# Kernel tuning notes

Measured on AMD Instinct MI355X. Metric: run time of the kernel, lower is better.

Reference implementation:

```python
import jax, jax.numpy as jnp
import numpy as np

B, E, H, W, HEADS = 2, 128, 64, 64, 4
FUSED = 2 * E + 1          # concat fusion: C_state + C_trigger + 1 (gnn context)
FC = FUSED // 2            # 128 fusion output channels (= AttentionMIL feature_dim)
EPS = 1e-5
NEG = -1e9


def _conv(x, w, b=None, pad=0):
    out = jax.lax.conv_general_dilated(x, w, (1, 1), [(pad, pad), (pad, pad)],
                                       dimension_numbers=('NCHW', 'OIHW', 'NCHW'))
    return out if b is None else out + b[None, :, None, None]


def _bn(x, g, b):
    # training-mode batchnorm (batch statistics), matching torch default mode
    m = x.mean((0, 2, 3), keepdims=True)
    v = x.var((0, 2, 3), keepdims=True)
    return g[None, :, None, None] * (x - m) * jax.lax.rsqrt(v + EPS) + b[None, :, None, None]


def _mha(q_in, kv_in, w_qkv, b_qkv, w_out, b_out, nheads):
    Bq, L, Em = q_in.shape
    d = Em // nheads
    wq, wk, wv = jnp.split(w_qkv, 3, axis=0)
    bq, bk, bv = jnp.split(b_qkv, 3, axis=0)
    q = (q_in @ wq.T + bq).reshape(Bq, L, nheads, d)
    k = (kv_in @ wk.T + bk).reshape(Bq, -1, nheads, d)
    v = (kv_in @ wv.T + bv).reshape(Bq, -1, nheads, d)
    scores = jnp.einsum('bqhd,bkhd->bhqk', q, k) / jnp.sqrt(jnp.asarray(d, q.dtype))
    attn = jax.nn.softmax(scores, axis=-1)
    out = jnp.einsum('bhqk,bkhd->bqhd', attn, v).reshape(Bq, L, Em)
    return out @ w_out.T + b_out


def setup_inputs() -> dict:
    key = jax.random.key(0)
    ks = jax.random.split(key, 24)
    n = lambda k, s: jax.random.normal(k, s, jnp.float32)
    p = lambda k, s: 0.02 * jax.random.normal(k, s, jnp.float32)
    return dict(
        state_features=n(ks[0], (B, E, H, W)),
        trigger_features=n(ks[1], (B, E, H, W)),
        gnn_context=n(ks[2], (B, 1, H, W)),
        zone_patches=jax.random.randint(ks[3], (B, H, W), 0, 16).astype(jnp.int32),
        cats=jax.random.randint(ks[4], (B,), 0, 16).astype(jnp.int32),
        labels=jax.random.uniform(ks[5], (B,), jnp.float32),
        s2t_qkv_w=p(ks[6], (3 * E, E)), s2t_qkv_b=p(ks[7], (3 * E,)),
        s2t_out_w=p(ks[8], (E, E)), s2t_out_b=p(ks[9], (E,)),
        t2s_qkv_w=p(ks[10], (3 * E, E)), t2s_qkv_b=p(ks[11], (3 * E,)),
        t2s_out_w=p(ks[12], (E, E)), t2s_out_b=p(ks[13], (E,)),
        fconv1_w=p(ks[14], (FC, FUSED, 3, 3)),
        fbn1_g=jnp.ones((FC,), jnp.float32), fbn1_b=jnp.zeros((FC,), jnp.float32),
        fconv2_w=p(ks[15], (FC, FC, 3, 3)),
        fbn2_g=jnp.ones((FC,), jnp.float32), fbn2_b=jnp.zeros((FC,), jnp.float32),
        outc_w=p(ks[16], (1, FC, 1, 1)), outc_b=p(ks[17], (1,)),
        attn1_w=p(ks[18], (128, FC, 1, 1)), attn1_b=p(ks[19], (128,)),
        attn2_w=p(ks[20], (1, 128, 1, 1)), attn2_b=p(ks[21], (1,)),
    )


def reference(state_features, trigger_features, gnn_context, zone_patches, cats, labels,
              s2t_qkv_w, s2t_qkv_b, s2t_out_w, s2t_out_b,
              t2s_qkv_w, t2s_qkv_b, t2s_out_w, t2s_out_b,
              fconv1_w, fbn1_g, fbn1_b, fconv2_w, fbn2_g, fbn2_b,
              outc_w, outc_b, attn1_w, attn1_b, attn2_w, attn2_b):
    Bs = state_features.shape[0]
    # ---- CrossAttentionFusion ----
    sf = state_features.reshape(Bs, E, H * W).transpose(0, 2, 1)    # (B, HW, E)
    tf = trigger_features.reshape(Bs, E, H * W).transpose(0, 2, 1)
    s2t = _mha(sf, tf, s2t_qkv_w, s2t_qkv_b, s2t_out_w, s2t_out_b, HEADS)
    t2s = _mha(tf, sf, t2s_qkv_w, t2s_qkv_b, t2s_out_w, t2s_out_b, HEADS)
    s2t = s2t.transpose(0, 2, 1).reshape(Bs, E, H, W)
    t2s = t2s.transpose(0, 2, 1).reshape(Bs, E, H, W)
    fused = jnp.concatenate([s2t, t2s, gnn_context], axis=1)        # (B, 257, H, W)
    x = jax.nn.relu(_bn(_conv(fused, fconv1_w, pad=1), fbn1_g, fbn1_b))
    feat = jax.nn.relu(_bn(_conv(x, fconv2_w, pad=1), fbn2_g, fbn2_b))  # (B, FC, H, W)
    # ---- pixel logit head (decoder outc) ----
    pixel_logits = _conv(feat, outc_w, outc_b)[:, 0]                # (B, H, W)
    # ---- AttentionMIL (vectorized over batch) ----
    a = jax.nn.relu(_conv(feat, attn1_w, attn1_b))
    scores = _conv(a, attn2_w, attn2_b)[:, 0]                       # (B, H, W)
    mask = (zone_patches == cats[:, None, None]) & (zone_patches > 0)
    has = mask.any((1, 2))
    masked = jnp.where(mask, scores, NEG)                           # score*1 on valid, -1e9 elsewhere
    wts = jax.nn.softmax(masked.reshape(Bs, -1), axis=-1).reshape(Bs, H, W)
    attention_maps = jnp.where(has[:, None, None], wts, 0.0)
    bag = (pixel_logits * wts * mask.astype(wts.dtype)).sum((1, 2))
    bag = jnp.where(has, bag, 0.0)
    # BCEWithLogitsLoss(mean): softplus(x) - x*y
    loss = jnp.mean(jax.nn.softplus(bag) - bag * labels)
    return loss, attention_maps
```

## Files before the change

### kernel.cpp

```cpp
#include <hip/hip_runtime.h>
#include <hip/hip_bf16.h>
#include <math.h>

#define L 4096
#define ECH 128
#define BCH 2
#define NHEAD 4
#define FUSEDC 257
#define CPAD 288

typedef __attribute__((ext_vector_type(8))) short bs8;
typedef __attribute__((ext_vector_type(4))) short bs4;
typedef __attribute__((ext_vector_type(4))) float fx4;

#define SCL 0.25503518f

static __device__ __forceinline__ short f2bfs(float x) {
  unsigned u = __float_as_uint(x);
  u += 0x7fffu + ((u >> 16) & 1u);
  return (short)(u >> 16);
}

static __device__ __forceinline__ float bf2f(short s) {
  return __uint_as_float((unsigned)(unsigned short)s << 16);
}

static __device__ __forceinline__ float exp2a(float x) {
  float r; asm("v_exp_f32 %0, %1" : "=v"(r) : "v"(x)); return r;
}

static __device__ __forceinline__ unsigned pk2(float lo, float hi) {
  unsigned r; asm("v_cvt_pk_bf16_f32 %0, %1, %2" : "=v"(r) : "v"(lo), "v"(hi)); return r;
}

__global__ void transpose_kernel(const float* __restrict__ sf, const float* __restrict__ tf,
                                 short* __restrict__ Xs, short* __restrict__ Xt) {
  __shared__ float t[32][33];
  int z = blockIdx.z; int b = z & 1; int sel = z >> 1;
  const float* in = sel ? tf : sf;
  short* out = sel ? Xt : Xs;
  int bx = blockIdx.x * 32;
  int by = blockIdx.y * 32;
  int tx = threadIdx.x & 31, ty = threadIdx.x >> 5;
  const float* ip = in + (size_t)b * ECH * L;
  short* op = out + (size_t)b * L * ECH;
#pragma unroll
  for (int r = ty; r < 32; r += 8)
    t[r][tx] = ip[(size_t)(by + r) * L + bx + tx];
  __syncthreads();
#pragma unroll
  for (int r = ty; r < 32; r += 8)
    op[(size_t)(bx + r) * ECH + by + tx] = f2bfs(t[tx][r]);
}

__global__ void prep_all(const float* __restrict__ c1w, const float* __restrict__ c2w,
                         const float* __restrict__ wS, const float* __restrict__ wT,
                         const float* __restrict__ woS, const float* __restrict__ woT,
                         short* __restrict__ W1b, short* __restrict__ W2b,
                         short* __restrict__ wSb, short* __restrict__ wTb,
                         short* __restrict__ woSb, short* __restrict__ woTb) {
  int i = blockIdx.x * 256 + threadIdx.x;
  if (i < 331776) {
    int ci = i % CPAD; int rest = i / CPAD; int co = rest & 127; int tap = rest >> 7;
    W1b[i] = (ci < FUSEDC) ? f2bfs(c1w[(co * FUSEDC + ci) * 9 + tap]) : (short)0;
  } else if (i < 479232) {
    int j = i - 331776;
    int ci = j & 127; int co = (j >> 7) & 127; int tap = j >> 14;
    W2b[j] = f2bfs(c2w[(co * 128 + ci) * 9 + tap]);
  } else {
    int k = i - 479232;
    float s = (k < 16384) ? SCL : 1.0f;
    wSb[k] = f2bfs(wS[k] * s);
    wTb[k] = f2bfs(wT[k] * s);
    if (k < 16384) {
      woSb[k] = f2bfs(woS[k]);
      woTb[k] = f2bfs(woT[k]);
    }
  }
}

__global__ void __launch_bounds__(256)
gemm_qkv(const short* __restrict__ Xs, const short* __restrict__ Xt,
         const short* __restrict__ wSb, const short* __restrict__ wTb,
         const float* __restrict__ bS, const float* __restrict__ bT,
         short* __restrict__ qs, short* __restrict__ ks,
         short* __restrict__ qt, short* __restrict__ kt,
         short* __restrict__ vTs, short* __restrict__ vTt) {
  int unit = blockIdx.y;
  const short* X; const short* W; const float* bias; short* out; float scale; int mode;
  switch (unit) {
    case 0: X = Xs; W = wSb;         bias = bS;       out = qs;  scale = SCL; mode = 0; break;
    case 1: X = Xt; W = wSb + 16384; bias = bS + 128; out = ks;  scale = 1.f; mode = 1; break;
    case 2: X = Xt; W = wTb;         bias = bT;       out = qt;  scale = SCL; mode = 0; break;
    case 3: X = Xs; W = wTb + 16384; bias = bT + 128; out = kt;  scale = 1.f; mode = 1; break;
    case 4: X = Xt; W = wSb + 32768; bias = bS + 256; out = vTs; scale = 1.f; mode = 2; break;
    default:X = Xs; W = wTb + 32768; bias = bT + 256; out = vTt; scale = 1.f; mode = 2; break;
  }
  int tid = threadIdx.x;
  int wv = tid >> 6, lane = tid & 63, u = lane >> 4, r = lane & 15;
  int pblk = blockIdx.x * 64 + wv * 16;
  const short* xrow = X + (size_t)(pblk + r) * 128;
  fx4 acc[8] = {};
  if (mode != 2) {
#pragma unroll
    for (int ksx = 0; ksx < 4; ++ksx) {
      int k0 = ksx * 32 + u * 8;
      bs8 a = *(const bs8*)(xrow + k0);
      const short* wp = W + (size_t)r * 128 + k0;
#pragma unroll
      for (int t = 0; t < 8; ++t) {
        bs8 wf = *(const bs8*)(wp + (size_t)t * 16 * 128);
        acc[t] = __builtin_amdgcn_mfma_f32_16x16x32_bf16(a, wf, acc[t], 0, 0, 0);
      }
    }
  } else {
#pragma unroll
    for (int ksx = 0; ksx < 4; ++ksx) {
      int k0 = ksx * 32 + u * 8;
      bs8 xb = *(const bs8*)(xrow + k0);
      const short* wp = W + (size_t)r * 128 + k0;
#pragma unroll
      for (int t = 0; t < 8; ++t) {
        bs8 wf = *(const bs8*)(wp + (size_t)t * 16 * 128);
        acc[t] = __builtin_amdgcn_mfma_f32_16x16x32_bf16(wf, xb, acc[t], 0, 0, 0);
      }
    }
  }
  if (mode == 0) {
#pragma unroll
    for (int t = 0; t < 8; ++t) {
      float bv = bias[t * 16 + r] * scale;
#pragma unroll
      for (int reg = 0; reg < 4; ++reg) {
        int p = pblk + u * 4 + reg;
        out[(size_t)p * 128 + t * 16 + r] = f2bfs(acc[t][reg] + bv);
      }
    }
  } else if (mode == 1) {
#pragma unroll
    for (int t = 0; t < 8; ++t) {
      int och = t * 16 + r, h = och >> 5, d = och & 31;
      float bv = bias[och];
#pragma unroll
      for (int reg = 0; reg < 4; ++reg) {
        int p = pblk + u * 4 + reg;
        int b = p >> 12, pl = p & 4095;
        out[(((size_t)(b * NHEAD + h) * L + pl) << 5) + d] = f2bfs(acc[t][reg] + bv);
      }
    }
  } else {
    int p = pblk + r;
    int b = p >> 12, pl = p & 4095;
#pragma unroll
    for (int t = 0; t < 8; ++t) {
#pragma unroll
      for (int reg = 0; reg < 4; ++reg) {
        int och = t * 16 + u * 4 + reg;
        int h = och >> 5, d = och & 31;
        out[((size_t)(b * NHEAD + h) * 32 + d) * L + pl] = f2bfs(acc[t][reg] + bias[och]);
      }
    }
  }
}

__global__ void __launch_bounds__(256)
gemm_o(const short* __restrict__ aosb, const short* __restrict__ aotb,
       const short* __restrict__ woSb, const short* __restrict__ woTb,
       const float* __restrict__ boS, const float* __restrict__ boT,
       const float* __restrict__ gnn, short* __restrict__ fusedPM) {
  int unit = blockIdx.y;
  const short* X = unit ? aotb : aosb;
  const short* W = unit ? woTb : woSb;
  const float* bias = unit ? boT : boS;
  int ochbase = unit ? 128 : 0;
  int tid = threadIdx.x;
  int wv = tid >> 6, lane = tid & 63, u = lane >> 4, r = lane & 15;
  int pblk = blockIdx.x * 64 + wv * 16;
  const short* xrow = X + (size_t)(pblk + r) * 128;
  fx4 acc[8] = {};
#pragma unroll
  for (int ksx = 0; ksx < 4; ++ksx) {
    int k0 = ksx * 32 + u * 8;
    bs8 a = *(const bs8*)(xrow + k0);
    const short* wp = W + (size_t)r * 128 + k0;
#pragma unroll
    for (int t = 0; t < 8; ++t) {
      bs8 wf = *(const bs8*)(wp + (size_t)t * 16 * 128);
      acc[t] = __builtin_amdgcn_mfma_f32_16x16x32_bf16(a, wf, acc[t], 0, 0, 0);
    }
  }
#pragma unroll
  for (int t = 0; t < 8; ++t) {
    float bv = bias[t * 16 + r];
#pragma unroll
    for (int reg = 0; reg < 4; ++reg) {
      int p = pblk + u * 4 + reg;
      fusedPM[(size_t)p * CPAD + ochbase + t * 16 + r] = f2bfs(acc[t][reg] + bv);
    }
  }
  if (unit == 0) {
    int base = blockIdx.x * 64;
    for (int t2 = tid; t2 < 64 * 32; t2 += 256) {
      int p = base + (t2 >> 5), j = t2 & 31;
      fusedPM[(size_t)p * CPAD + 256 + j] = (j == 0) ? f2bfs(gnn[p]) : (short)0;
    }
  }
}

__global__ void __launch_bounds__(256, 4)
flash_attn6(const short* __restrict__ Qs, const short* __restrict__ Ks, const short* __restrict__ Vs,
            const short* __restrict__ Qt, const short* __restrict__ Kt, const short* __restrict__ Vt,
            short* __restrict__ poS, short* __restrict__ poT,
            float* __restrict__ pmS, float* __restrict__ plS,
            float* __restrict__ pmT, float* __restrict__ plT) {
  int z = blockIdx.z;
  int sp = z >> 2, att = (z >> 1) & 1, b = z & 1;
  const short* Q = att ? Qt : Qs;
  const short* K = att ? Kt : Ks;
  const short* VT = att ? Vt : Vs;
  short* po = att ? poT : poS;
  float* pm = att ? pmT : pmS;
  float* pl = att ? plT : plS;
  int tid = threadIdx.x;
  int wid = tid >> 6, lane = tid & 63;
  int u = lane >> 4, r = lane & 15;
  int h = blockIdx.y;
  int qt0 = (blockIdx.x << 4) + (wid << 2);
  bs8 qf0 = *(const bs8*)(Q + ((size_t)(b * L + ((qt0 + 0) << 4) + r) * 128 + h * 32 + u * 8));
  bs8 qf1 = *(const bs8*)(Q + ((size_t)(b * L + ((qt0 + 1) << 4) + r) * 128 + h * 32 + u * 8));
  bs8 qf2 = *(const bs8*)(Q + ((size_t)(b * L + ((qt0 + 2) << 4) + r) * 128 + h * 32 + u * 8));
  bs8 qf3 = *(const bs8*)(Q + ((size_t)(b * L + ((qt0 + 3) << 4) + r) * 128 + h * 32 + u * 8));
  const short* Kb = K + (((size_t)(b * NHEAD + h) * L + sp * 1024) << 5) + u * 8;
  const short* Vb = VT + ((size_t)(b * NHEAD + h) * 32) * (size_t)L + sp * 1024;
  const short* v0p = Vb + (size_t)r * L + (u << 2);
  const short* v1p = Vb + (size_t)(16 + r) * L + (u << 2);
  fx4 o0[4] = {}, o1[4] = {};
  float l[4] = {0.f, 0.f, 0.f, 0.f};
  float m = -1.0e30f;
#pragma unroll 1
  for (int k0 = 0; k0 < 1024; k0 += 64) {
    bs8 a0 = *(const bs8*)(Kb + (((size_t)(k0 + r)) << 5));
    bs8 a1 = *(const bs8*)(Kb + (((size_t)(k0 + 16 + r)) << 5));
    bs8 a2 = *(const bs8*)(Kb + (((size_t)(k0 + 32 + r)) << 5));
    bs8 a3 = *(const bs8*)(Kb + (((size_t)(k0 + 48 + r)) << 5));
    bs4 w0 = *(const bs4*)(v0p + k0);
    bs4 w1 = *(const bs4*)(v0p + k0 + 16);
    bs4 w2 = *(const bs4*)(v0p + k0 + 32);
    bs4 w3 = *(const bs4*)(v0p + k0 + 48);
    bs4 w4 = *(const bs4*)(v1p + k0);
    bs4 w5 = *(const bs4*)(v1p + k0 + 16);
    bs4 w6 = *(const bs4*)(v1p + k0 + 32);
    bs4 w7 = *(const bs4*)(v1p + k0 + 48);
    bs8 vb0lo = __builtin_shufflevector(w0, w1, 0, 1, 2, 3, 4, 5, 6, 7);
    bs8 vb0hi = __builtin_shufflevector(w2, w3, 0, 1, 2, 3, 4, 5, 6, 7);
    bs8 vb1lo = __builtin_shufflevector(w4, w5, 0, 1, 2, 3, 4, 5, 6, 7);
    bs8 vb1hi = __builtin_shufflevector(w6, w7, 0, 1, 2, 3, 4, 5, 6, 7);
    fx4 zz = {0.f, 0.f, 0.f, 0.f};
#pragma unroll
    for (int t = 0; t < 4; ++t) {
      bs8 qf = (t == 0) ? qf0 : (t == 1) ? qf1 : (t == 2) ? qf2 : qf3;
      fx4 s0 = __builtin_amdgcn_mfma_f32_16x16x32_bf16(a0, qf, zz, 0, 0, 0);
      fx4 s1 = __builtin_amdgcn_mfma_f32_16x16x32_bf16(a1, qf, zz, 0, 0, 0);
      fx4 s2 = __builtin_amdgcn_mfma_f32_16x16x32_bf16(a2, qf, zz, 0, 0, 0);
      fx4 s3 = __builtin_amdgcn_mfma_f32_16x16x32_bf16(a3, qf, zz, 0, 0, 0);
      float mx = fmaxf(fmaxf(fmaxf(s0[0], s0[1]), fmaxf(s0[2], s0[3])),
                       fmaxf(fmaxf(s1[0], s1[1]), fmaxf(s1[2], s1[3])));
      mx = fmaxf(mx, fmaxf(fmaxf(fmaxf(s2[0], s2[1]), fmaxf(s2[2], s2[3])),
                           fmaxf(fmaxf(s3[0], s3[1]), fmaxf(s3[2], s3[3]))));
      if (!__all(mx <= m + 8.0f)) {
        float gm = fmaxf(mx, __shfl_xor(mx, 1));
        gm = fmaxf(gm, __shfl_xor(gm, 2));
        gm = fmaxf(gm, __shfl_xor(gm, 4));
        gm = fmaxf(gm, __shfl_xor(gm, 8));
        gm = fmaxf(gm, __shfl_xor(gm, 16));
        gm = fmaxf(gm, __shfl_xor(gm, 32));
        float m_new = fmaxf(m, gm);
        float fsc = exp2a(m - m_new);
#pragma unroll
        for (int tt = 0; tt < 4; ++tt) {
          l[tt] *= fsc;
#pragma unroll
          for (int rg = 0; rg < 4; ++rg) { o0[tt][rg] *= fsc; o1[tt][rg] *= fsc; }
        }
        m = m_new;
      }
      fx4 p0, p1, p2, p3;
#pragma unroll
      for (int i = 0; i < 4; ++i) {
        p0[i] = exp2a(s0[i] - m);
        p1[i] = exp2a(s1[i] - m);
        p2[i] = exp2a(s2[i] - m);
        p3[i] = exp2a(s3[i] - m);
      }
      l[t] += ((p0[0] + p0[1]) + (p0[2] + p0[3])) + ((p1[0] + p1[1]) + (p1[2] + p1[3]))
            + ((p2[0] + p2[1]) + (p2[2] + p2[3])) + ((p3[0] + p3[1]) + (p3[2] + p3[3]));
      union { unsigned w32[4]; bs8 v; } plo, phi;
      plo.w32[0] = pk2(p0[0], p0[1]); plo.w32[1] = pk2(p0[2], p0[3]);
      plo.w32[2] = pk2(p1[0], p1[1]); plo.w32[3] = pk2(p1[2], p1[3]);
      phi.w32[0] = pk2(p2[0], p2[1]); phi.w32[1] = pk2(p2[2], p2[3]);
      phi.w32[2] = pk2(p3[0], p3[1]); phi.w32[3] = pk2(p3[2], p3[3]);
      o0[t] = __builtin_amdgcn_mfma_f32_16x16x32_bf16(plo.v, vb0lo, o0[t], 0, 0, 0);
      o0[t] = __builtin_amdgcn_mfma_f32_16x16x32_bf16(phi.v, vb0hi, o0[t], 0, 0, 0);
      o1[t] = __builtin_amdgcn_mfma_f32_16x16x32_bf16(plo.v, vb1lo, o1[t], 0, 0, 0);
      o1[t] = __builtin_amdgcn_mfma_f32_16x16x32_bf16(phi.v, vb1hi, o1[t], 0, 0, 0);
    }
  }
#pragma unroll
  for (int t = 0; t < 4; ++t) {
    float lt = l[t];
    lt += __shfl_xor(lt, 16);
    lt += __shfl_xor(lt, 32);
    int rowb = ((b * NHEAD + h) << 12) + ((qt0 + t) << 4);
    if (lane < 16) {
      pm[(sp << 15) + rowb + r] = m;
      pl[(sp << 15) + rowb + r] = lt;
    }
#pragma unroll
    for (int reg = 0; reg < 4; ++reg) {
      size_t ob = ((size_t)sp << 20) + ((size_t)(rowb + (u << 2) + reg) << 5);
      po[ob + r] = f2bfs(o0[t][reg]);
      po[ob + 16 + r] = f2bfs(o1[t][reg]);
    }
  }
}

__global__ void combine_attn(const short* __restrict__ poS, const float* __restrict__ pmS,
                             const float* __restrict__ plS,
                             const short* __restrict__ poT, const float* __restrict__ pmT,
                             const float* __restrict__ plT,
                             short* __restrict__ aos, short* __restrict__ aot) {
  int i = blockIdx.x * 256 + threadIdx.x;
  int att = i >> 20, j = i & 0xFFFFF;
  const short* po = att ? poT : poS;
  const float* pm = att ? pmT : pmS;
  const float* pl = att ? plT : plS;
  short* out = att ? aot : aos;
  int row = j >> 5, d = j & 31;
  float m0 = pm[row], m1 = pm[32768 + row];
  float m2 = pm[65536 + row], m3 = pm[98304 + row];
  float l0 = pl[row], l1 = pl[32768 + row];
  float l2 = pl[65536 + row], l3 = pl[98304 + row];
  float m = fmaxf(fmaxf(m0, m1), fmaxf(m2, m3));
  float f0 = exp2f(m0 - m), f1 = exp2f(m1 - m);
  float f2 = exp2f(m2 - m), f3 = exp2f(m3 - m);
  float v0 = bf2f(po[j]);
  float v1 = bf2f(po[(1 << 20) + j]);
  float v2 = bf2f(po[(2 << 20) + j]);
  float v3 = bf2f(po[(3 << 20) + j]);
  float num = v0 * f0 + v1 * f1 + v2 * f2 + v3 * f3;
  float den = l0 * f0 + l1 * f1 + l2 * f2 + l3 * f3;
  float val = num / den;
  int q = row & 4095, h = (row >> 12) & 3, b = row >> 14;
  out[(((size_t)(b << 12) + q) << 7) + (h << 5) + d] = f2bfs(val);
}

__global__ void __launch_bounds__(128)
conv1_mfma(const short* __restrict__ X, const short* __restrict__ W,
           float* __restrict__ out) {
  int tid = threadIdx.x;
  int wv = tid >> 6, lane = tid & 63, u = lane >> 4, r = lane & 15;
  int pblk = blockIdx.x * 32 + wv * 16;
  int ybase = blockIdx.y * 32;
  int b = pblk >> 12, y = (pblk & 4095) >> 6, x0 = pblk & 63;
  fx4 acc[2] = {};
  for (int tap = 0; tap < 9; ++tap) {
    int dy = tap / 3 - 1, dx = tap % 3 - 1;
    int yy = y + dy;
    if (yy < 0 || yy > 63) { __syncthreads(); continue; }
    int xx = x0 + r + dx;
    bool valid = (xx >= 0) && (xx <= 63);
    const short* xrow = X + (size_t)((b << 12) + (yy << 6) + x0 + dx + r) * CPAD;
    const short* wtap = W + ((size_t)tap * 128 + ybase + r) * CPAD;
#pragma unroll
    for (int kc = 0; kc < 9; ++kc) {
      int k0 = kc * 32 + u * 8;
      bs8 a = {};
      if (valid) a = *(const bs8*)(xrow + k0);
#pragma unroll
      for (int t = 0; t < 2; ++t) {
        bs8 wf = *(const bs8*)(wtap + (size_t)t * 16 * CPAD + k0);
        acc[t] = __builtin_amdgcn_mfma_f32_16x16x32_bf16(a, wf, acc[t], 0, 0, 0);
      }
    }
    __syncthreads();
  }
#pragma unroll
  for (int t = 0; t < 2; ++t)
#pragma unroll
    for (int reg = 0; reg < 4; ++reg)
      out[(size_t)(pblk + u * 4 + reg) * 128 + ybase + t * 16 + r] = acc[t][reg];
}

__global__ void __launch_bounds__(128)
conv2_mfma(const short* __restrict__ X, const short* __restrict__ W,
           float* __restrict__ out) {
  int tid = threadIdx.x;
  int wv = tid >> 6, lane = tid & 63, u = lane >> 4, r = lane & 15;
  int pblk = blockIdx.x * 32 + wv * 16;
  int ybase = blockIdx.y * 32;
  int b = pblk >> 12, y = (pblk & 4095) >> 6, x0 = pblk & 63;
  fx4 acc[2] = {};
  for (int tap = 0; tap < 9; ++tap) {
    int dy = tap / 3 - 1, dx = tap % 3 - 1;
    int yy = y + dy;
    if (yy < 0 || yy > 63) { __syncthreads(); continue; }
    int xx = x0 + r + dx;
    bool valid = (xx >= 0) && (xx <= 63);
    const short* xrow = X + (size_t)((b << 12) + (yy << 6) + x0 + dx + r) * 128;
    const short* wtap = W + ((size_t)tap * 128 + ybase + r) * 128;
#pragma unroll
    for (int kc = 0; kc < 4; ++kc) {
      int k0 = kc * 32 + u * 8;
      bs8 xb = {};
      if (valid) xb = *(const bs8*)(xrow + k0);
#pragma unroll
      for (int t = 0; t < 2; ++t) {
        bs8 wf = *(const bs8*)(wtap + (size_t)t * 16 * 128 + k0);
        acc[t] = __builtin_amdgcn_mfma_f32_16x16x32_bf16(wf, xb, acc[t], 0, 0, 0);
      }
    }
    __syncthreads();
  }
  int px = y * 64 + x0 + r;
#pragma unroll
  for (int t = 0; t < 2; ++t)
#pragma unroll
    for (int reg = 0; reg < 4; ++reg) {
      int och = ybase + t * 16 + u * 4 + reg;
      out[((size_t)(b * 128 + och) << 12) + px] = acc[t][reg];
    }
}

__global__ void bnstats_pm(const float* __restrict__ x, float* __restrict__ mean,
                           float* __restrict__ rstd) {
  __shared__ float rs[256], rq[256];
  int c = blockIdx.x, tid = threadIdx.x;
  float s = 0, q = 0;
  for (int p = tid; p < BCH * L; p += 256) {
    float v = x[(size_t)p * 128 + c];
    s += v; q += v * v;
  }
  rs[tid] = s; rq[tid] = q; __syncthreads();
  for (int st = 128; st > 0; st >>= 1) { if (tid < st) { rs[tid] += rs[tid + st]; rq[tid] += rq[tid + st]; } __syncthreads(); }
  if (tid == 0) {
    float m = rs[0] / (float)(BCH * L);
    float v = rq[0] / (float)(BCH * L) - m * m;
    mean[c] = m;
    rstd[c] = rsqrtf(v + 1e-5f);
  }
}

__global__ void bnapply_pm(const float* __restrict__ x, const float* __restrict__ mean,
                           const float* __restrict__ rstd, const float* __restrict__ g,
                           const float* __restrict__ bb, short* __restrict__ out) {
  int i = blockIdx.x * 256 + threadIdx.x;
  int c = i & 127;
  float v = x[i];
  out[i] = f2bfs(fmaxf(g[c] * (v - mean[c]) * rstd[c] + bb[c], 0.0f));
}

__global__ void bnstats_kernel(const float* __restrict__ x, float* __restrict__ mean, float* __restrict__ rstd) {
  __shared__ float rs[256], rq[256];
  int c = blockIdx.x, tid = threadIdx.x;
  float s = 0, q = 0;
  for (int i = tid; i < BCH * L; i += 256) {
    int b = i >> 12, p = i & 4095;
    float v = x[((size_t)(b * 128 + c)) * L + p];
    s += v; q += v * v;
  }
  rs[tid] = s; rq[tid] = q; __syncthreads();
  for (int st = 128; st > 0; st >>= 1) { if (tid < st) { rs[tid] += rs[tid + st]; rq[tid] += rq[tid + st]; } __syncthreads(); }
  if (tid == 0) {
    float m = rs[0] / (float)(BCH * L);
    float v = rq[0] / (float)(BCH * L) - m * m;
    mean[c] = m;
    rstd[c] = rsqrtf(v + 1e-5f);
  }
}

__global__ void head_kernel(const float* __restrict__ feat,
                            const float* __restrict__ bmean, const float* __restrict__ brstd,
                            const float* __restrict__ bg, const float* __restrict__ bbias,
                            const float* __restrict__ w1, const float* __restrict__ b1,
                            const float* __restrict__ w2, const float* __restrict__ b2,
                            const float* __restrict__ wo, const float* __restrict__ bo,
                            float* __restrict__ score, float* __restrict__ plog) {
  __shared__ float f[128][64];
  __shared__ float r1[4][64], r2[4][64];
  int by = blockIdx.x; int b = by >> 6, y = by & 63;
  int tid = threadIdx.x;
  int x = tid & 63, g4 = tid >> 6;
  for (int c = g4; c < 128; c += 4) {
    float v = feat[((size_t)(b * 128 + c)) * L + y * 64 + x];
    f[c][x] = fmaxf(bg[c] * (v - bmean[c]) * brstd[c] + bbias[c], 0.0f);
  }
  __syncthreads();
  int cb = g4 * 32;
  float a[32];
#pragma unroll
  for (int i = 0; i < 32; ++i) a[i] = b1[cb + i];
  for (int ci = 0; ci < 128; ++ci) {
    float fv = f[ci][x];
#pragma unroll
    for (int i = 0; i < 32; ++i) a[i] += w1[(size_t)(cb + i) * 128 + ci] * fv;
  }
  float sp = 0.0f;
#pragma unroll
  for (int i = 0; i < 32; ++i) sp += w2[cb + i] * fmaxf(a[i], 0.0f);
  float plp = 0.0f;
#pragma unroll
  for (int i = 0; i < 32; ++i) plp += wo[cb + i] * f[cb + i][x];
  r1[g4][x] = sp; r2[g4][x] = plp;
  __syncthreads();
  if (tid < 64) {
    int xx = tid;
    float s = r1[0][xx] + r1[1][xx] + r1[2][xx] + r1[3][xx] + b2[0];
    float pl = r2[0][xx] + r2[1][xx] + r2[2][xx] + r2[3][xx] + bo[0];
    score[(size_t)b * L + y * 64 + xx] = s;
    plog[(size_t)b * L + y * 64 + xx] = pl;
  }
}

__global__ void finalize_kernel(const float* __restrict__ score, const float* __restrict__ plog,
                                const int* __restrict__ zone, const int* __restrict__ cats,
                                float* __restrict__ maps, float* __restrict__ bag_ws) {
  __shared__ float sc[4096];
  __shared__ float red[256];
  __shared__ int ired[256];
  int b = blockIdx.x, tid = threadIdx.x;
  int cat = cats[b];
  float lmax = -3e38f; int lhas = 0;
  for (int p = tid; p < 4096; p += 256) {
    int z = zone[(size_t)b * 4096 + p];
    int m = (z == cat) && (z > 0);
    float s = m ? score[(size_t)b * 4096 + p] : -1e9f;
    sc[p] = s; lmax = fmaxf(lmax, s); lhas |= m;
  }
  red[tid] = lmax; ired[tid] = lhas; __syncthreads();
  for (int st = 128; st > 0; st >>= 1) {
    if (tid < st) { red[tid] = fmaxf(red[tid], red[tid + st]); ired[tid] |= ired[tid + st]; }
    __syncthreads();
  }
  float gmax = red[0]; int has = ired[0];
  __syncthreads();
  float lsum = 0;
  for (int p = tid; p < 4096; p += 256) {
    float e = __expf(sc[p] - gmax);
    sc[p] = e; lsum += e;
  }
  red[tid] = lsum; __syncthreads();
  for (int st = 128; st > 0; st >>= 1) { if (tid < st) red[tid] += red[tid + st]; __syncthreads(); }
  float inv = 1.0f / red[0];
  __syncthreads();
  float lbag = 0;
  for (int p = tid; p < 4096; p += 256) {
    float w = sc[p] * inv;
    maps[(size_t)b * 4096 + p] = has ? w : 0.0f;
    int z = zone[(size_t)b * 4096 + p];
    if ((z == cat) && (z > 0)) lbag += plog[(size_t)b * 4096 + p] * w;
  }
  red[tid] = lbag; __syncthreads();
  for (int st = 128; st > 0; st >>= 1) { if (tid < st) red[tid] += red[tid + st]; __syncthreads(); }
  if (tid == 0) bag_ws[b] = has ? red[0] : 0.0f;
}

__global__ void loss_kernel(const float* __restrict__ bag_ws, const float* __restrict__ labels,
                            float* __restrict__ out) {
  if (threadIdx.x == 0 && blockIdx.x == 0) {
    float t = 0;
    for (int b = 0; b < BCH; ++b) {
      float x = bag_ws[b];
      float sp = fmaxf(x, 0.0f) + log1pf(expf(-fabsf(x)));
      t += sp - x * labels[b];
    }
    out[0] = t / (float)BCH;
  }
}

extern "C" void kernel_launch(void* const* d_in, const int* in_sizes, int n_in,
                              void* d_out, int out_size, void* d_ws, size_t ws_size,
                              hipStream_t stream) {
  (void)in_sizes; (void)n_in; (void)out_size; (void)ws_size;
  const float* state = (const float*)d_in[0];
  const float* trig  = (const float*)d_in[1];
  const float* gnn   = (const float*)d_in[2];
  const int*   zone  = (const int*)d_in[3];
  const int*   cats  = (const int*)d_in[4];
  const float* labels = (const float*)d_in[5];
  const float* s2t_qkv_w = (const float*)d_in[6];
  const float* s2t_qkv_b = (const float*)d_in[7];
  const float* s2t_out_w = (const float*)d_in[8];
  const float* s2t_out_b = (const float*)d_in[9];
  const float* t2s_qkv_w = (const float*)d_in[10];
  const float* t2s_qkv_b = (const float*)d_in[11];
  const float* t2s_out_w = (const float*)d_in[12];
  const float* t2s_out_b = (const float*)d_in[13];
  const float* fconv1_w = (const float*)d_in[14];
  const float* fbn1_g = (const float*)d_in[15];
  const float* fbn1_b = (const float*)d_in[16];
  const float* fconv2_w = (const float*)d_in[17];
  const float* fbn2_g = (const float*)d_in[18];
  const float* fbn2_b = (const float*)d_in[19];
  const float* outc_w = (const float*)d_in[20];
  const float* outc_b = (const float*)d_in[21];
  const float* attn1_w = (const float*)d_in[22];
  const float* attn1_b = (const float*)d_in[23];
  const float* attn2_w = (const float*)d_in[24];
  const float* attn2_b = (const float*)d_in[25];

  float* ws = (float*)d_ws;
  const size_t NBP = (size_t)BCH * L * 128;
  size_t o = 0;
  float* c1 = ws + o; o += NBP;
  float* c2 = ws + o; o += NBP;
  float* stats = ws + o; o += 512;
  float* score = ws + o; o += (size_t)BCH * L;
  float* plog = ws + o; o += (size_t)BCH * L;
  float* bag = ws + o; o += 8;
  short* Xs = (short*)(ws + o); o += NBP / 2;
  short* Xt = (short*)(ws + o); o += NBP / 2;
  short* qsb = (short*)(ws + o); o += NBP / 2;
  short* ksb = (short*)(ws + o); o += NBP / 2;
  short* qtb = (short*)(ws + o); o += NBP / 2;
  short* ktb = (short*)(ws + o); o += NBP / 2;
  short* vTsb = (short*)(ws + o); o += NBP / 2;
  short* vTtb = (short*)(ws + o); o += NBP / 2;
  short* aosb = (short*)(ws + o); o += NBP / 2;
  short* aotb = (short*)(ws + o); o += NBP / 2;
  short* fusedPM = (short*)(ws + o); o += (size_t)BCH * L * CPAD / 2;
  short* X2 = (short*)(ws + o); o += NBP / 2;
  short* W1b = (short*)(ws + o); o += (9 * 128 * CPAD) / 2;
  short* W2b = (short*)(ws + o); o += (9 * 128 * 128) / 2;
  short* wSb = (short*)(ws + o); o += 24576;
  short* wTb = (short*)(ws + o); o += 24576;
  short* woSb = (short*)(ws + o); o += 8192;
  short* woTb = (short*)(ws + o); o += 8192;
  short* poT = (short*)(ws + o); o += 2 * NBP;

  short* poS = (short*)c1;
  float* pmS = (float*)fusedPM;
  float* plS = pmS + 131072;
  float* pmT = plS + 131072;
  float* plT = pmT + 131072;

  prep_all<<<2064, 256, 0, stream>>>(fconv1_w, fconv2_w, s2t_qkv_w, t2s_qkv_w,
                                     s2t_out_w, t2s_out_w,
                                     W1b, W2b, wSb, wTb, woSb, woTb);
  transpose_kernel<<<dim3(128, 4, 2 * BCH), 256, 0, stream>>>(state, trig, Xs, Xt);

  gemm_qkv<<<dim3(128, 6), 256, 0, stream>>>(Xs, Xt, wSb, wTb, s2t_qkv_b, t2s_qkv_b,
                                             qsb, ksb, qtb, ktb, vTsb, vTtb);

  flash_attn6<<<dim3(16, NHEAD, 16), 256, 0, stream>>>(qsb, ksb, vTsb, qtb, ktb, vTtb,
                                                       poS, poT, pmS, plS, pmT, plT);
  combine_attn<<<8192, 256, 0, stream>>>(poS, pmS, plS, poT, pmT, plT, aosb, aotb);

  gemm_o<<<dim3(128, 2), 256, 0, stream>>>(aosb, aotb, woSb, woTb, s2t_out_b, t2s_out_b,
                                           gnn, fusedPM);

  conv1_mfma<<<dim3(256, 4), 128, 0, stream>>>(fusedPM, W1b, c1);
  bnstats_pm<<<128, 256, 0, stream>>>(c1, stats, stats + 128);
  bnapply_pm<<<4096, 256, 0, stream>>>(c1, stats, stats + 128, fbn1_g, fbn1_b, X2);

  conv2_mfma<<<dim3(256, 4), 128, 0, stream>>>(X2, W2b, c2);
  bnstats_kernel<<<128, 256, 0, stream>>>(c2, stats + 256, stats + 384);

  head_kernel<<<BCH * 64, 256, 0, stream>>>(c2, stats + 256, stats + 384, fbn2_g, fbn2_b,
                                            attn1_w, attn1_b, attn2_w, attn2_b,
                                            outc_w, outc_b, score, plog);

  finalize_kernel<<<BCH, 256, 0, stream>>>(score, plog, zone, cats, (float*)d_out + 1, bag);
  loss_kernel<<<1, 64, 0, stream>>>(bag, labels, (float*)d_out);
}
```

Baseline: 276.8 us.

## Fuse BN statistics into conv epilogues and merge prep with transpose

The conv1 and conv2 MFMA kernels now reduce per-channel sum and sum-of-squares across their output tile using wave shuffles and write partial results to a slot buffer. A small stats_reduce kernel then folds the 512 partials per channel, replacing the old batchnorm stats kernels that re-read the full conv outputs (conv1 output read with a 128-float stride). Weight preparation and input transposition are also merged into one launch. The change adds shuffle work and extra partial-sum stores to the conv epilogues and enlarges the workspace.

```diff
diff --git a/kernel.cpp b/kernel.cpp
--- a/kernel.cpp
+++ b/kernel.cpp
@@ -33,49 +33,52 @@
   unsigned r; asm("v_cvt_pk_bf16_f32 %0, %1, %2" : "=v"(r) : "v"(lo), "v"(hi)); return r;
 }
 
-__global__ void transpose_kernel(const float* __restrict__ sf, const float* __restrict__ tf,
-                                 short* __restrict__ Xs, short* __restrict__ Xt) {
+__global__ void prep_fused(const float* __restrict__ c1w, const float* __restrict__ c2w,
+                           const float* __restrict__ wS, const float* __restrict__ wT,
+                           const float* __restrict__ woS, const float* __restrict__ woT,
+                           const float* __restrict__ sf, const float* __restrict__ tf,
+                           short* __restrict__ W1b, short* __restrict__ W2b,
+                           short* __restrict__ wSb, short* __restrict__ wTb,
+                           short* __restrict__ woSb, short* __restrict__ woTb,
+                           short* __restrict__ Xs, short* __restrict__ Xt) {
   __shared__ float t[32][33];
-  int z = blockIdx.z; int b = z & 1; int sel = z >> 1;
-  const float* in = sel ? tf : sf;
-  short* out = sel ? Xt : Xs;
-  int bx = blockIdx.x * 32;
-  int by = blockIdx.y * 32;
-  int tx = threadIdx.x & 31, ty = threadIdx.x >> 5;
-  const float* ip = in + (size_t)b * ECH * L;
-  short* op = out + (size_t)b * L * ECH;
-#pragma unroll
-  for (int r = ty; r < 32; r += 8)
-    t[r][tx] = ip[(size_t)(by + r) * L + bx + tx];
-  __syncthreads();
-#pragma unroll
-  for (int r = ty; r < 32; r += 8)
-    op[(size_t)(bx + r) * ECH + by + tx] = f2bfs(t[tx][r]);
-}
-
-__global__ void prep_all(const float* __restrict__ c1w, const float* __restrict__ c2w,
-                         const float* __restrict__ wS, const float* __restrict__ wT,
-                         const float* __restrict__ woS, const float* __restrict__ woT,
-                         short* __restrict__ W1b, short* __restrict__ W2b,
-                         short* __restrict__ wSb, short* __restrict__ wTb,
-                         short* __restrict__ woSb, short* __restrict__ woTb) {
-  int i = blockIdx.x * 256 + threadIdx.x;
-  if (i < 331776) {
-    int ci = i % CPAD; int rest = i / CPAD; int co = rest & 127; int tap = rest >> 7;
-    W1b[i] = (ci < FUSEDC) ? f2bfs(c1w[(co * FUSEDC + ci) * 9 + tap]) : (short)0;
-  } else if (i < 479232) {
-    int j = i - 331776;
-    int ci = j & 127; int co = (j >> 7) & 127; int tap = j >> 14;
-    W2b[j] = f2bfs(c2w[(co * 128 + ci) * 9 + tap]);
+  int bid = blockIdx.x;
+  if (bid < 2064) {
+    int i = bid * 256 + threadIdx.x;
+    if (i < 331776) {
+      int ci = i % CPAD; int rest = i / CPAD; int co = rest & 127; int tap = rest >> 7;
+      W1b[i] = (ci < FUSEDC) ? f2bfs(c1w[(co * FUSEDC + ci) * 9 + tap]) : (short)0;
+    } else if (i < 479232) {
+      int j = i - 331776;
+      int ci = j & 127; int co = (j >> 7) & 127; int tap = j >> 14;
+      W2b[j] = f2bfs(c2w[(co * 128 + ci) * 9 + tap]);
+    } else {
+      int k = i - 479232;
+      float s = (k < 16384) ? SCL : 1.0f;
+      wSb[k] = f2bfs(wS[k] * s);
+      wTb[k] = f2bfs(wT[k] * s);
+      if (k < 16384) {
+        woSb[k] = f2bfs(woS[k]);
+        woTb[k] = f2bfs(woT[k]);
+      }
+    }
   } else {
-    int k = i - 479232;
-    float s = (k < 16384) ? SCL : 1.0f;
-    wSb[k] = f2bfs(wS[k] * s);
-    wTb[k] = f2bfs(wT[k] * s);
-    if (k < 16384) {
-      woSb[k] = f2bfs(woS[k]);
-      woTb[k] = f2bfs(woT[k]);
-    }
+    int id = bid - 2064;
+    int bx = (id & 127) * 32;
+    int by = ((id >> 7) & 3) * 32;
+    int z = id >> 9; int b = z & 1; int sel = z >> 1;
+    const float* in = sel ? tf : sf;
+    short* out = sel ? Xt : Xs;
+    int tx = threadIdx.x & 31, ty = threadIdx.x >> 5;
+    const float* ip = in + (size_t)b * ECH * L;
+    short* op = out + (size_t)b * L * ECH;
+#pragma unroll
+    for (int r = ty; r < 32; r += 8)
+      t[r][tx] = ip[(size_t)(by + r) * L + bx + tx];
+    __syncthreads();
+#pragma unroll
+    for (int r = ty; r < 32; r += 8)
+      op[(size_t)(bx + r) * ECH + by + tx] = f2bfs(t[tx][r]);
   }
 }
 
@@ -356,7 +359,7 @@
 
 __global__ void __launch_bounds__(128)
 conv1_mfma(const short* __restrict__ X, const short* __restrict__ W,
-           float* __restrict__ out) {
+           float* __restrict__ out, float* __restrict__ psum, float* __restrict__ psq) {
   int tid = threadIdx.x;
   int wv = tid >> 6, lane = tid & 63, u = lane >> 4, r = lane & 15;
   int pblk = blockIdx.x * 32 + wv * 16;
@@ -385,15 +388,26 @@
     __syncthreads();
   }
 #pragma unroll
-  for (int t = 0; t < 2; ++t)
+  for (int t = 0; t < 2; ++t) {
 #pragma unroll
     for (int reg = 0; reg < 4; ++reg)
       out[(size_t)(pblk + u * 4 + reg) * 128 + ybase + t * 16 + r] = acc[t][reg];
+    float s = (acc[t][0] + acc[t][1]) + (acc[t][2] + acc[t][3]);
+    float q = (acc[t][0] * acc[t][0] + acc[t][1] * acc[t][1])
+            + (acc[t][2] * acc[t][2] + acc[t][3] * acc[t][3]);
+    s += __shfl_xor(s, 16); s += __shfl_xor(s, 32);
+    q += __shfl_xor(q, 16); q += __shfl_xor(q, 32);
+    if (u == 0) {
+      int slot = (ybase + t * 16 + r) * 512 + blockIdx.x * 2 + wv;
+      psum[slot] = s;
+      psq[slot] = q;
+    }
+  }
 }
 
 __global__ void __launch_bounds__(128)
 conv2_mfma(const short* __restrict__ X, const short* __restrict__ W,
-           float* __restrict__ out) {
+           float* __restrict__ out, float* __restrict__ psum, float* __restrict__ psq) {
   int tid = threadIdx.x;
   int wv = tid >> 6, lane = tid & 63, u = lane >> 4, r = lane & 15;
   int pblk = blockIdx.x * 32 + wv * 16;
@@ -423,28 +437,43 @@
   }
   int px = y * 64 + x0 + r;
 #pragma unroll
-  for (int t = 0; t < 2; ++t)
+  for (int t = 0; t < 2; ++t) {
 #pragma unroll
     for (int reg = 0; reg < 4; ++reg) {
       int och = ybase + t * 16 + u * 4 + reg;
       out[((size_t)(b * 128 + och) << 12) + px] = acc[t][reg];
     }
-}
-
-__global__ void bnstats_pm(const float* __restrict__ x, float* __restrict__ mean,
-                           float* __restrict__ rstd) {
+#pragma unroll
+    for (int reg = 0; reg < 4; ++reg) {
+      float s = acc[t][reg];
+      float q = s * s;
+      s += __shfl_xor(s, 1); q += __shfl_xor(q, 1);
+      s += __shfl_xor(s, 2); q += __shfl_xor(q, 2);
+      s += __shfl_xor(s, 4); q += __shfl_xor(q, 4);
+      s += __shfl_xor(s, 8); q += __shfl_xor(q, 8);
+      if (r == 0) {
+        int slot = (ybase + t * 16 + u * 4 + reg) * 512 + blockIdx.x * 2 + wv;
+        psum[slot] = s;
+        psq[slot] = q;
+      }
+    }
+  }
+}
+
+__global__ void stats_reduce(const float* __restrict__ psum, const float* __restrict__ psq,
+                             float* __restrict__ mean, float* __restrict__ rstd) {
   __shared__ float rs[256], rq[256];
   int c = blockIdx.x, tid = threadIdx.x;
-  float s = 0, q = 0;
-  for (int p = tid; p < BCH * L; p += 256) {
-    float v = x[(size_t)p * 128 + c];
-    s += v; q += v * v;
-  }
+  float s = psum[c * 512 + tid] + psum[c * 512 + 256 + tid];
+  float q = psq[c * 512 + tid] + psq[c * 512 + 256 + tid];
   rs[tid] = s; rq[tid] = q; __syncthreads();
-  for (int st = 128; st > 0; st >>= 1) { if (tid < st) { rs[tid] += rs[tid + st]; rq[tid] += rq[tid + st]; } __syncthreads(); }
+  for (int st = 128; st > 0; st >>= 1) {
+    if (tid < st) { rs[tid] += rs[tid + st]; rq[tid] += rq[tid + st]; }
+    __syncthreads();
+  }
   if (tid == 0) {
-    float m = rs[0] / (float)(BCH * L);
-    float v = rq[0] / (float)(BCH * L) - m * m;
+    float m = rs[0] / 8192.0f;
+    float v = rq[0] / 8192.0f - m * m;
     mean[c] = m;
     rstd[c] = rsqrtf(v + 1e-5f);
   }
@@ -457,25 +486,6 @@
   int c = i & 127;
   float v = x[i];
   out[i] = f2bfs(fmaxf(g[c] * (v - mean[c]) * rstd[c] + bb[c], 0.0f));
-}
-
-__global__ void bnstats_kernel(const float* __restrict__ x, float* __restrict__ mean, float* __restrict__ rstd) {
-  __shared__ float rs[256], rq[256];
-  int c = blockIdx.x, tid = threadIdx.x;
-  float s = 0, q = 0;
-  for (int i = tid; i < BCH * L; i += 256) {
-    int b = i >> 12, p = i & 4095;
-    float v = x[((size_t)(b * 128 + c)) * L + p];
-    s += v; q += v * v;
-  }
-  rs[tid] = s; rq[tid] = q; __syncthreads();
-  for (int st = 128; st > 0; st >>= 1) { if (tid < st) { rs[tid] += rs[tid + st]; rq[tid] += rq[tid + st]; } __syncthreads(); }
-  if (tid == 0) {
-    float m = rs[0] / (float)(BCH * L);
-    float v = rq[0] / (float)(BCH * L) - m * m;
-    mean[c] = m;
-    rstd[c] = rsqrtf(v + 1e-5f);
-  }
 }
 
 __global__ void head_kernel(const float* __restrict__ feat,
@@ -636,6 +646,10 @@
   short* woSb = (short*)(ws + o); o += 8192;
   short* woTb = (short*)(ws + o); o += 8192;
   short* poT = (short*)(ws + o); o += 2 * NBP;
+  float* psum1 = ws + o; o += 128 * 512;
+  float* psq1 = ws + o; o += 128 * 512;
+  float* psum2 = ws + o; o += 128 * 512;
+  float* psq2 = ws + o; o += 128 * 512;
 
   short* poS = (short*)c1;
   float* pmS = (float*)fusedPM;
@@ -643,10 +657,9 @@
   float* pmT = plS + 131072;
   float* plT = pmT + 131072;
 
-  prep_all<<<2064, 256, 0, stream>>>(fconv1_w, fconv2_w, s2t_qkv_w, t2s_qkv_w,
-                                     s2t_out_w, t2s_out_w,
-                                     W1b, W2b, wSb, wTb, woSb, woTb);
-  transpose_kernel<<<dim3(128, 4, 2 * BCH), 256, 0, stream>>>(state, trig, Xs, Xt);
+  prep_fused<<<4112, 256, 0, stream>>>(fconv1_w, fconv2_w, s2t_qkv_w, t2s_qkv_w,
+                                       s2t_out_w, t2s_out_w, state, trig,
+                                       W1b, W2b, wSb, wTb, woSb, woTb, Xs, Xt);
 
   gemm_qkv<<<dim3(128, 6), 256, 0, stream>>>(Xs, Xt, wSb, wTb, s2t_qkv_b, t2s_qkv_b,
                                              qsb, ksb, qtb, ktb, vTsb, vTtb);
@@ -658,12 +671,12 @@
   gemm_o<<<dim3(128, 2), 256, 0, stream>>>(aosb, aotb, woSb, woTb, s2t_out_b, t2s_out_b,
                                            gnn, fusedPM);
 
-  conv1_mfma<<<dim3(256, 4), 128, 0, stream>>>(fusedPM, W1b, c1);
-  bnstats_pm<<<128, 256, 0, stream>>>(c1, stats, stats + 128);
+  conv1_mfma<<<dim3(256, 4), 128, 0, stream>>>(fusedPM, W1b, c1, psum1, psq1);
+  stats_reduce<<<128, 256, 0, stream>>>(psum1, psq1, stats, stats + 128);
   bnapply_pm<<<4096, 256, 0, stream>>>(c1, stats, stats + 128, fbn1_g, fbn1_b, X2);
 
-  conv2_mfma<<<dim3(256, 4), 128, 0, stream>>>(X2, W2b, c2);
-  bnstats_kernel<<<128, 256, 0, stream>>>(c2, stats + 256, stats + 384);
+  conv2_mfma<<<dim3(256, 4), 128, 0, stream>>>(X2, W2b, c2, psum2, psq2);
+  stats_reduce<<<128, 256, 0, stream>>>(psum2, psq2, stats + 256, stats + 384);
 
   head_kernel<<<BCH * 64, 256, 0, stream>>>(c2, stats + 256, stats + 384, fbn2_g, fbn2_b,
                                             attn1_w, attn1_b, attn2_w, attn2_b,
```

New measurement: 255.5 us. -7.7%, faster.
